# Optimization experiments

Hardware: AMD Instinct MI355X
Metric: run time of the kernel (lower is better)

Reference implementation:

```python
import jax, jax.numpy as jnp
import numpy as np

NUM_HEADS = 16

def setup_inputs() -> dict:
    key = jax.random.key(0)
    k1, k2, k3, k4, k5 = jax.random.split(key, 5)
    B, N, C = 4, 2048, 1024
    N2, Cy = 1024, 768
    x = jax.random.normal(k1, (B, N, C), dtype=jnp.float32)
    y = jax.random.normal(k2, (B, N2, Cy), dtype=jnp.float32)
    pad_mask = jax.random.randint(k3, (B, N), 0, 2).astype(jnp.bool_)
    # Linear weights (torch convention: out = inp @ W.T), scaled ~ fan-in init
    Wq = jax.random.normal(k4, (C, C), dtype=jnp.float32) * (C ** -0.5)
    Wkv = jax.random.normal(k5, (2 * C, Cy), dtype=jnp.float32) * (Cy ** -0.5)
    return {"x": x, "y": y, "pad_mask": pad_mask, "Wq": Wq, "Wkv": Wkv}


def reference(x, y, pad_mask, Wq, Wkv):
    B, N, C = x.shape
    N2 = y.shape[1]
    H = NUM_HEADS
    d = C // H
    scale = d ** -0.5
    # q: [B, H, N, d]
    q = (x @ Wq.T).reshape(B, N, H, d).transpose(0, 2, 1, 3)
    # kv: [B, N2, 2, H, d] -> k, v each [B, H, N2, d]
    kv = (y @ Wkv.T).reshape(B, N2, 2, H, d).transpose(2, 0, 3, 1, 4)
    k, v = kv[0], kv[1]
    # scores: [B, H, N, N2]
    attn = jnp.einsum("bhnd,bhmd->bhnm", q * scale, k)
    # pad_mask is indexed by the QUERY axis and broadcast over keys (faithful
    # to the original einops.repeat 'B Q -> B H Q L'). False -> -1e9.
    attn = jnp.where(pad_mask[:, None, :, None], attn, jnp.float32(-1e9))
    attn = jax.nn.softmax(attn, axis=-1)
    out = jnp.einsum("bhnm,bhmd->bhnd", attn, v)  # [B, H, N, d]
    return out.transpose(0, 2, 1, 3).reshape(B, N, C)
```

## Files before the change

kernel.cpp:

```cpp
#include <hip/hip_runtime.h>

typedef unsigned short u16;
typedef unsigned int u32;
typedef __attribute__((ext_vector_type(8))) __bf16 bf16x8;
typedef __attribute__((ext_vector_type(4))) float f32x4;

__device__ __forceinline__ u16 f2bf(float f) {
  unsigned u = __float_as_uint(f);
  u += 0x7FFFu + ((u >> 16) & 1u);
  return (u16)(u >> 16);
}

__device__ __forceinline__ float fast_exp2(float x) { return __builtin_amdgcn_exp2f(x); }
__device__ __forceinline__ float fast_rcp(float x) { return __builtin_amdgcn_rcpf(x); }

__global__ void cvt_all(const float* __restrict__ x, const float* __restrict__ Wq,
                        const float* __restrict__ y, const float* __restrict__ Wkv,
                        const int* __restrict__ mask,
                        u16* __restrict__ Xb, u16* __restrict__ Wqb,
                        u16* __restrict__ Yb, u16* __restrict__ Wkvb) {
  int i = blockIdx.x * 256 + threadIdx.x;
  const float4* src;
  u16* dst;
  int j;
  float sc;
  if (i < 2097152) {
    j = i; src = (const float4*)x; dst = Xb;
    sc = (mask[i >> 8] != 0) ? 1.0f : 0.0f;
  } else if (i < 2359296) {
    j = i - 2097152; src = (const float4*)Wq; dst = Wqb;
    sc = 0.18033688f;
  } else if (i < 3145728) {
    j = i - 2359296; src = (const float4*)y; dst = Yb;
    sc = 1.0f;
  } else {
    j = i - 3145728; src = (const float4*)Wkv; dst = Wkvb;
    sc = 1.0f;
  }
  float4 v = src[j];
  ushort4 o;
  o.x = f2bf(v.x * sc);
  o.y = f2bf(v.y * sc);
  o.z = f2bf(v.z * sc);
  o.w = f2bf(v.w * sc);
  ((ushort4*)dst)[j] = o;
}

__global__ __launch_bounds__(256) void gemm_bt(const u16* __restrict__ A,
                                               const u16* __restrict__ B,
                                               u16* __restrict__ C,
                                               int M, int N, int K) {
  __shared__ __align__(16) u16 sA[128 * 32];
  __shared__ __align__(16) u16 sB[128 * 32];
  const int t = threadIdx.x;
  const int wave = t >> 6;
  const int lane = t & 63;
  const int wm = (wave >> 1) * 64;
  const int wn = (wave & 1) * 64;
  const int fr = lane & 15;
  const int quad = lane >> 4;
  const int fk = quad * 8;
  const int sr = lane >> 2;
  const int sc = (lane & 3) * 8;

  f32x4 acc[4][4];
  const f32x4 z4 = {0.f, 0.f, 0.f, 0.f};
#pragma unroll
  for (int i = 0; i < 4; ++i)
#pragma unroll
    for (int j = 0; j < 4; ++j) acc[i][j] = z4;

  const u16* Abase = A + (size_t)blockIdx.x * 128 * K;
  const u16* Bbase = B + (size_t)blockIdx.y * 128 * K;

  for (int k0 = 0; k0 < K; k0 += 32) {
#pragma unroll
    for (int q = 0; q < 2; ++q) {
      const int chunk = wave * 2 + q;
      const int row = chunk * 16 + sr;
      __builtin_amdgcn_global_load_lds(
          (__attribute__((address_space(1))) void*)(Abase + (size_t)row * K + k0 + sc),
          (__attribute__((address_space(3))) void*)(sA + chunk * 512), 16, 0, 0);
      __builtin_amdgcn_global_load_lds(
          (__attribute__((address_space(1))) void*)(Bbase + (size_t)row * K + k0 + sc),
          (__attribute__((address_space(3))) void*)(sB + chunk * 512), 16, 0, 0);
    }
    __syncthreads();
    bf16x8 af[4], bfv[4];
#pragma unroll
    for (int i = 0; i < 4; ++i)
      af[i] = *(const bf16x8*)(sA + (wm + i * 16 + fr) * 32 + fk);
#pragma unroll
    for (int j = 0; j < 4; ++j)
      bfv[j] = *(const bf16x8*)(sB + (wn + j * 16 + fr) * 32 + fk);
#pragma unroll
    for (int i = 0; i < 4; ++i)
#pragma unroll
      for (int j = 0; j < 4; ++j)
        acc[i][j] = __builtin_amdgcn_mfma_f32_16x16x32_bf16(af[i], bfv[j], acc[i][j], 0, 0, 0);
    __syncthreads();
  }

#pragma unroll
  for (int i = 0; i < 4; ++i)
#pragma unroll
    for (int j = 0; j < 4; ++j)
#pragma unroll
      for (int r = 0; r < 4; ++r) {
        const int row = blockIdx.x * 128 + wm + i * 16 + quad * 4 + r;
        const int col = blockIdx.y * 128 + wn + j * 16 + fr;
        C[(size_t)row * N + col] = f2bf(acc[i][j][r]);
      }
}

__global__ void transpose_v(const u16* __restrict__ KV, u16* __restrict__ Vt) {
  __shared__ u16 tile[64][66];
  const int t = threadIdx.x;
  const int rb = blockIdx.x * 64;
  const int h = blockIdx.y;
#pragma unroll
  for (int i = 0; i < 16; ++i) {
    int idx = i * 256 + t;
    int r = idx >> 6, c = idx & 63;
    tile[r][c] = KV[(size_t)(rb + r) * 2048 + 1024 + h * 64 + c];
  }
  __syncthreads();
  const int b = blockIdx.x >> 4;
  const int n2b = (blockIdx.x & 15) * 64;
#pragma unroll
  for (int i = 0; i < 16; ++i) {
    int idx = i * 256 + t;
    int dd = idx >> 6, n2 = idx & 63;
    int cperm = (n2 & 32) | (((n2 >> 2) & 3) << 3) | (((n2 >> 4) & 1) << 2) | (n2 & 3);
    Vt[(size_t)((b * 16 + h) * 64 + dd) * 1024 + n2b + cperm] = tile[n2][dd];
  }
}

__global__ __launch_bounds__(256, 2) void attn_kernel(
    const u16* __restrict__ Q, const u16* __restrict__ KV,
    const u16* __restrict__ Vt, float* __restrict__ Out) {
  __shared__ __align__(16) u16 sK[2 * 128 * 64];
  __shared__ __align__(16) u16 sV[2 * 64 * 128];
  __shared__ float red[4][2][4][16];

  const int t = threadIdx.x;
  const int wave = t >> 6;
  const int lane = t & 63;
  const int g = blockIdx.x & 63;
  const int qt = blockIdx.x >> 6;
  const int b = g >> 4;
  const int h = g & 15;
  const int q0 = qt * 128;
  const int fr = lane & 15;
  const int quad = lane >> 4;
  const int l3 = lane >> 3, l7 = lane & 7;
  const int l4 = lane >> 4, l15 = lane & 15;

  const u16* qbase = Q + (size_t)(b * 2048 + q0 + wave * 16 + fr) * 1024 + h * 64 + quad * 8;
  bf16x8 qa[2][2];
  qa[0][0] = *(const bf16x8*)(qbase);
  qa[0][1] = *(const bf16x8*)(qbase + 32);
  qa[1][0] = *(const bf16x8*)(qbase + (size_t)64 * 1024);
  qa[1][1] = *(const bf16x8*)(qbase + (size_t)64 * 1024 + 32);

  const int kq = (l7 ^ l3) * 8;
  auto stage = [&](int kcn, u16* dK, u16* dV) {
#pragma unroll
    for (int i = 0; i < 4; ++i) {
      const int j = wave * 4 + i;
      const u16* ksrc = KV + (size_t)(b * 1024 + kcn * 128 + 8 * j + l3) * 2048 + h * 64 + kq;
      __builtin_amdgcn_global_load_lds(
          (__attribute__((address_space(1))) void*)ksrc,
          (__attribute__((address_space(3))) void*)(dK + j * 512), 16, 0, 0);
      const int vq = (l15 ^ ((i & 1) * 4 + l4)) * 8;
      const u16* vsrc = Vt + (size_t)((b * 16 + h) * 64 + 4 * j + l4) * 1024 + kcn * 128 + vq;
      __builtin_amdgcn_global_load_lds(
          (__attribute__((address_space(1))) void*)vsrc,
          (__attribute__((address_space(3))) void*)(dV + j * 512), 16, 0, 0);
    }
  };

  stage(0, sK, sV);
  __syncthreads();

  const f32x4 z4 = {0.f, 0.f, 0.f, 0.f};
  f32x4 o[2][4];
  float l_run[2] = {0.f, 0.f};
#pragma unroll
  for (int hh = 0; hh < 2; ++hh)
#pragma unroll
    for (int nt = 0; nt < 4; ++nt) o[hh][nt] = z4;

  const int f7 = fr & 7;
  const int ck0 = (quad ^ f7) * 8;
  const int ck1 = ((quad ^ 4) ^ f7) * 8;

  for (int kc = 0; kc < 8; ++kc) {
    const u16* sKc = sK + (kc & 1) * 8192;
    const u16* sVc = sV + (kc & 1) * 8192;
    if (kc < 7) stage(kc + 1, sK + ((kc + 1) & 1) * 8192, sV + ((kc + 1) & 1) * 8192);

#pragma unroll
    for (int ks = 0; ks < 4; ++ks) {
      f32x4 s0[2], s1[2];
      {
        const u16* kb = sKc + ((2 * ks) * 16 + fr) * 64;
        bf16x8 k0 = *(const bf16x8*)(kb + ck0);
        bf16x8 k1 = *(const bf16x8*)(kb + ck1);
        s0[0] = __builtin_amdgcn_mfma_f32_16x16x32_bf16(k0, qa[0][0], z4, 0, 0, 0);
        s0[0] = __builtin_amdgcn_mfma_f32_16x16x32_bf16(k1, qa[0][1], s0[0], 0, 0, 0);
        s0[1] = __builtin_amdgcn_mfma_f32_16x16x32_bf16(k0, qa[1][0], z4, 0, 0, 0);
        s0[1] = __builtin_amdgcn_mfma_f32_16x16x32_bf16(k1, qa[1][1], s0[1], 0, 0, 0);
      }
      {
        const u16* kb = sKc + ((2 * ks + 1) * 16 + fr) * 64;
        bf16x8 k0 = *(const bf16x8*)(kb + ck0);
        bf16x8 k1 = *(const bf16x8*)(kb + ck1);
        s1[0] = __builtin_amdgcn_mfma_f32_16x16x32_bf16(k0, qa[0][0], z4, 0, 0, 0);
        s1[0] = __builtin_amdgcn_mfma_f32_16x16x32_bf16(k1, qa[0][1], s1[0], 0, 0, 0);
        s1[1] = __builtin_amdgcn_mfma_f32_16x16x32_bf16(k0, qa[1][0], z4, 0, 0, 0);
        s1[1] = __builtin_amdgcn_mfma_f32_16x16x32_bf16(k1, qa[1][1], s1[1], 0, 0, 0);
      }

      bf16x8 pa[2];
#pragma unroll
      for (int hh = 0; hh < 2; ++hh) {
        f32x4& a = (hh == 0) ? s0[0] : s0[1];
        f32x4& bb = (hh == 0) ? s1[0] : s1[1];
        float l = 0.f;
#pragma unroll
        for (int r = 0; r < 4; ++r) {
          float p0 = fast_exp2(a[r]); a[r] = p0; l += p0;
          float p1 = fast_exp2(bb[r]); bb[r] = p1; l += p1;
        }
        l_run[hh] += l;
        bf16x8 pv;
        pv[0] = (__bf16)a[0];  pv[1] = (__bf16)a[1];
        pv[2] = (__bf16)a[2];  pv[3] = (__bf16)a[3];
        pv[4] = (__bf16)bb[0]; pv[5] = (__bf16)bb[1];
        pv[6] = (__bf16)bb[2]; pv[7] = (__bf16)bb[3];
        pa[hh] = pv;
      }

#pragma unroll
      for (int ntd = 0; ntd < 4; ++ntd) {
        const int cv = (((ks * 4 + quad) ^ f7)) * 8;
        bf16x8 vb = *(const bf16x8*)(sVc + (ntd * 16 + fr) * 128 + cv);
        o[0][ntd] = __builtin_amdgcn_mfma_f32_16x16x32_bf16(pa[0], vb, o[0][ntd], 0, 0, 0);
        o[1][ntd] = __builtin_amdgcn_mfma_f32_16x16x32_bf16(pa[1], vb, o[1][ntd], 0, 0, 0);
      }
    }

    if (kc < 7) __syncthreads();
  }

  red[wave][0][quad][fr] = l_run[0];
  red[wave][1][quad][fr] = l_run[1];
  __syncthreads();

#pragma unroll
  for (int hh = 0; hh < 2; ++hh) {
    float inv[4];
#pragma unroll
    for (int r = 0; r < 4; ++r) {
      const int ql = quad * 4 + r;
      float d = red[wave][hh][0][ql] + red[wave][hh][1][ql] +
                red[wave][hh][2][ql] + red[wave][hh][3][ql];
      inv[r] = fast_rcp(d);
    }
#pragma unroll
    for (int ntd = 0; ntd < 4; ++ntd)
#pragma unroll
      for (int r = 0; r < 4; ++r) {
        const int row = q0 + hh * 64 + wave * 16 + quad * 4 + r;
        const int col = h * 64 + ntd * 16 + fr;
        Out[(size_t)(b * 2048 + row) * 1024 + col] = o[hh][ntd][r] * inv[r];
      }
  }
}

extern "C" void kernel_launch(void* const* d_in, const int* in_sizes, int n_in,
                              void* d_out, int out_size, void* d_ws, size_t ws_size,
                              hipStream_t stream) {
  (void)in_sizes; (void)n_in; (void)out_size; (void)ws_size;
  const float* x   = (const float*)d_in[0];
  const float* y   = (const float*)d_in[1];
  const int*   msk = (const int*)d_in[2];
  const float* Wq  = (const float*)d_in[3];
  const float* Wkv = (const float*)d_in[4];
  float* out = (float*)d_out;

  char* ws = (char*)d_ws;
  const size_t MB = 1024 * 1024;
  u16* Xb   = (u16*)(ws + 0);
  u16* Wqb  = (u16*)(ws + 16 * MB);
  u16* Yb   = (u16*)(ws + 18 * MB);
  u16* Wkvb = (u16*)(ws + 24 * MB);
  u16* Qb   = (u16*)(ws + 27 * MB);
  u16* KVb  = (u16*)(ws + 0);
  u16* Vtb  = (u16*)(ws + 43 * MB);

  cvt_all<<<13824, 256, 0, stream>>>(x, Wq, y, Wkv, msk, Xb, Wqb, Yb, Wkvb);
  gemm_bt<<<dim3(64, 8), 256, 0, stream>>>(Xb, Wqb, Qb, 8192, 1024, 1024);
  gemm_bt<<<dim3(32, 16), 256, 0, stream>>>(Yb, Wkvb, KVb, 4096, 2048, 768);
  transpose_v<<<dim3(64, 16), 256, 0, stream>>>(KVb, Vtb);
  attn_kernel<<<1024, 256, 0, stream>>>(Qb, KVb, Vtb, out);
}
```

Baseline: 198.6 us.

## Merge Q and KV projection GEMMs into one launch with double-buffered LDS

The two projection GEMMs are combined into a single kernel launch, with the block index selecting the Q or KV problem. This fills the GPU with 1024 blocks at once and removes one launch and its tail. The K loop now double-buffers the LDS tiles, issuing the next tile's global-to-LDS loads before computing on the current one, and drops one barrier per iteration. The KV output buffer is moved so it no longer aliases the X buffer, since both GEMMs now run concurrently. The larger LDS footprint may reduce occupancy.

```diff
diff --git a/kernel.cpp b/kernel.cpp
--- a/kernel.cpp
+++ b/kernel.cpp
@@ -46,12 +46,11 @@
   ((ushort4*)dst)[j] = o;
 }
 
-__global__ __launch_bounds__(256) void gemm_bt(const u16* __restrict__ A,
-                                               const u16* __restrict__ B,
-                                               u16* __restrict__ C,
-                                               int M, int N, int K) {
-  __shared__ __align__(16) u16 sA[128 * 32];
-  __shared__ __align__(16) u16 sB[128 * 32];
+__global__ __launch_bounds__(256) void gemm_dual(
+    const u16* __restrict__ Aq, const u16* __restrict__ Bq, u16* __restrict__ Cq,
+    const u16* __restrict__ Akv, const u16* __restrict__ Bkv, u16* __restrict__ Ckv) {
+  __shared__ __align__(16) u16 sA[2 * 128 * 32];
+  __shared__ __align__(16) u16 sB[2 * 128 * 32];
   const int t = threadIdx.x;
   const int wave = t >> 6;
   const int lane = t & 63;
@@ -63,6 +62,19 @@
   const int sr = lane >> 2;
   const int sc = (lane & 3) * 8;
 
+  const u16 *A, *B;
+  u16* C;
+  int N, K, bx, by;
+  const int blk = blockIdx.x;
+  if (blk < 512) {
+    A = Aq; B = Bq; C = Cq; N = 1024; K = 1024;
+    bx = blk >> 3; by = blk & 7;
+  } else {
+    A = Akv; B = Bkv; C = Ckv; N = 2048; K = 768;
+    const int id = blk - 512;
+    bx = id >> 4; by = id & 15;
+  }
+
   f32x4 acc[4][4];
   const f32x4 z4 = {0.f, 0.f, 0.f, 0.f};
 #pragma unroll
@@ -70,35 +82,46 @@
 #pragma unroll
     for (int j = 0; j < 4; ++j) acc[i][j] = z4;
 
-  const u16* Abase = A + (size_t)blockIdx.x * 128 * K;
-  const u16* Bbase = B + (size_t)blockIdx.y * 128 * K;
-
-  for (int k0 = 0; k0 < K; k0 += 32) {
+  const u16* Abase = A + (size_t)bx * 128 * K;
+  const u16* Bbase = B + (size_t)by * 128 * K;
+
+  auto stage = [&](int k0, u16* dA, u16* dB) {
 #pragma unroll
     for (int q = 0; q < 2; ++q) {
       const int chunk = wave * 2 + q;
       const int row = chunk * 16 + sr;
       __builtin_amdgcn_global_load_lds(
           (__attribute__((address_space(1))) void*)(Abase + (size_t)row * K + k0 + sc),
-          (__attribute__((address_space(3))) void*)(sA + chunk * 512), 16, 0, 0);
+          (__attribute__((address_space(3))) void*)(dA + chunk * 512), 16, 0, 0);
       __builtin_amdgcn_global_load_lds(
           (__attribute__((address_space(1))) void*)(Bbase + (size_t)row * K + k0 + sc),
-          (__attribute__((address_space(3))) void*)(sB + chunk * 512), 16, 0, 0);
+          (__attribute__((address_space(3))) void*)(dB + chunk * 512), 16, 0, 0);
     }
-    __syncthreads();
+  };
+
+  stage(0, sA, sB);
+  __syncthreads();
+
+  int it = 0;
+  for (int k0 = 0; k0 < K; k0 += 32, ++it) {
+    u16* cA = sA + (it & 1) * 4096;
+    u16* cB = sB + (it & 1) * 4096;
+    if (k0 + 32 < K) stage(k0 + 32, sA + ((it + 1) & 1) * 4096, sB + ((it + 1) & 1) * 4096);
+
     bf16x8 af[4], bfv[4];
 #pragma unroll
     for (int i = 0; i < 4; ++i)
-      af[i] = *(const bf16x8*)(sA + (wm + i * 16 + fr) * 32 + fk);
+      af[i] = *(const bf16x8*)(cA + (wm + i * 16 + fr) * 32 + fk);
 #pragma unroll
     for (int j = 0; j < 4; ++j)
-      bfv[j] = *(const bf16x8*)(sB + (wn + j * 16 + fr) * 32 + fk);
+      bfv[j] = *(const bf16x8*)(cB + (wn + j * 16 + fr) * 32 + fk);
 #pragma unroll
     for (int i = 0; i < 4; ++i)
 #pragma unroll
       for (int j = 0; j < 4; ++j)
         acc[i][j] = __builtin_amdgcn_mfma_f32_16x16x32_bf16(af[i], bfv[j], acc[i][j], 0, 0, 0);
-    __syncthreads();
+
+    if (k0 + 32 < K) __syncthreads();
   }
 
 #pragma unroll
@@ -107,8 +130,8 @@
     for (int j = 0; j < 4; ++j)
 #pragma unroll
       for (int r = 0; r < 4; ++r) {
-        const int row = blockIdx.x * 128 + wm + i * 16 + quad * 4 + r;
-        const int col = blockIdx.y * 128 + wn + j * 16 + fr;
+        const int row = bx * 128 + wm + i * 16 + quad * 4 + r;
+        const int col = by * 128 + wn + j * 16 + fr;
         C[(size_t)row * N + col] = f2bf(acc[i][j][r]);
       }
 }
@@ -297,12 +320,11 @@
   u16* Yb   = (u16*)(ws + 18 * MB);
   u16* Wkvb = (u16*)(ws + 24 * MB);
   u16* Qb   = (u16*)(ws + 27 * MB);
-  u16* KVb  = (u16*)(ws + 0);
-  u16* Vtb  = (u16*)(ws + 43 * MB);
+  u16* KVb  = (u16*)(ws + 43 * MB);
+  u16* Vtb  = (u16*)(ws + 59 * MB);
 
   cvt_all<<<13824, 256, 0, stream>>>(x, Wq, y, Wkv, msk, Xb, Wqb, Yb, Wkvb);
-  gemm_bt<<<dim3(64, 8), 256, 0, stream>>>(Xb, Wqb, Qb, 8192, 1024, 1024);
-  gemm_bt<<<dim3(32, 16), 256, 0, stream>>>(Yb, Wkvb, KVb, 4096, 2048, 768);
+  gemm_dual<<<1024, 256, 0, stream>>>(Xb, Wqb, Qb, Yb, Wkvb, KVb);
   transpose_v<<<dim3(64, 16), 256, 0, stream>>>(KVb, Vtb);
   attn_kernel<<<1024, 256, 0, stream>>>(Qb, KVb, Vtb, out);
 }
```

New measurement: 194.6 us. 1.02x faster.
